# Optimization experiments

Measured on AMD Instinct MI355X. Metric: run time of the kernel, lower is better.

## Reference

```python
import jax, jax.numpy as jnp
import numpy as np
import math

B, S, E = 4, 2048, 1024


def setup_inputs() -> dict:
    key = jax.random.key(0)
    ks = jax.random.split(key, 9)
    x = jax.random.normal(ks[0], (B, S, E), dtype=jnp.float32)
    # causal boolean mask, broadcast over batch: True = keep
    mask = jnp.broadcast_to(jnp.tril(jnp.ones((S, S), dtype=bool)), (B, S, S))
    sc = 1.0 / math.sqrt(E)
    Wq = jax.random.normal(ks[1], (E, E), dtype=jnp.float32) * sc
    bq = jnp.zeros((E,), dtype=jnp.float32)
    Wk = jax.random.normal(ks[2], (E, E), dtype=jnp.float32) * sc
    bk = jnp.zeros((E,), dtype=jnp.float32)
    Wv = jax.random.normal(ks[3], (E, E), dtype=jnp.float32) * sc
    bv = jnp.zeros((E,), dtype=jnp.float32)
    gamma = jnp.ones((E,), dtype=jnp.float32)
    beta = jnp.zeros((E,), dtype=jnp.float32)
    return {"x": x, "mask": mask, "Wq": Wq, "bq": bq, "Wk": Wk, "bk": bk,
            "Wv": Wv, "bv": bv, "gamma": gamma, "beta": beta}


def reference(x, mask, Wq, bq, Wk, bk, Wv, bv, gamma, beta):
    E_ = x.shape[-1]
    q = jnp.einsum('bse,fe->bsf', x, Wq) + bq
    k = jnp.einsum('bse,fe->bsf', x, Wk) + bk
    v = jnp.einsum('bse,fe->bsf', x, Wv) + bv
    scores = jnp.einsum('bqe,bke->bqk', q, k) / jnp.sqrt(jnp.float32(E_))
    scores = jnp.where(mask, scores, -jnp.inf)
    probs = jax.nn.softmax(scores, axis=-1)
    attn = jnp.einsum('bqk,bke->bqe', probs, v)
    y = attn + x
    # LayerNorm over last dim, eps matches torch default 1e-5
    mu = jnp.mean(y, axis=-1, keepdims=True)
    var = jnp.mean(jnp.square(y - mu), axis=-1, keepdims=True)
    return (y - mu) / jnp.sqrt(var + 1e-5) * gamma + beta
```

## Files before the change

kernel.cpp:

```cpp
#include <hip/hip_runtime.h>
#include <hip/hip_bf16.h>
#include <stdint.h>

#define B_ 4
#define S_ 2048
#define E_ 1024
#define BS_ (B_*S_)

using bf16x8 = __attribute__((ext_vector_type(8))) __bf16;
using f32x4  = __attribute__((ext_vector_type(4))) float;

__device__ __forceinline__ unsigned short f2bf(float f) {
  unsigned int u = __float_as_uint(f);
  u += 0x7fffu + ((u >> 16) & 1u);
  return (unsigned short)(u >> 16);
}

__device__ __forceinline__ void gld16(const unsigned short* g, unsigned short* l) {
  __builtin_amdgcn_global_load_lds((__attribute__((address_space(1))) void*)(void*)g,
                                   (__attribute__((address_space(3))) void*)l, 16, 0, 0);
}

__global__ __launch_bounds__(256) void conv_f32_bf16(const float* __restrict__ in,
                                                     unsigned short* __restrict__ out,
                                                     int n4) {
  int i = blockIdx.x * 256 + threadIdx.x;
  if (i >= n4) return;
  const float4 v = ((const float4*)in)[i];
  ushort4 o;
  o.x = f2bf(v.x); o.y = f2bf(v.y); o.z = f2bf(v.z); o.w = f2bf(v.w);
  ((ushort4*)out)[i] = o;
}

__global__ __launch_bounds__(256) void concat_bias(const float* __restrict__ a,
                                                   const float* __restrict__ b,
                                                   const float* __restrict__ c,
                                                   float* __restrict__ o) {
  int i = blockIdx.x * 256 + threadIdx.x;
  if (i >= 3 * E_) return;
  o[i] = (i < E_) ? a[i] : (i < 2 * E_ ? b[i - E_] : c[i - 2 * E_]);
}

template<int EPI>
__global__ __launch_bounds__(256, 2) void gemm_bt(
    const unsigned short* __restrict__ A, const unsigned short* __restrict__ Bm,
    float* __restrict__ Cf, unsigned short* __restrict__ Cb,
    const float* __restrict__ bias,
    int K, int lda, int ldb, int ldc,
    long sA, long sB, long sC, float scale, int causal)
{
  constexpr int BM = 128, BN = 128, BK = 64;
  __shared__ __align__(16) unsigned short As[BM * BK];
  __shared__ __align__(16) unsigned short Bs[BN * BK];
  const int bz = blockIdx.z;
  A  += sA * bz;
  Bm += sB * bz;
  const int m0 = blockIdx.y * BM, n0 = blockIdx.x * BN;
  if (EPI == 1 && causal && n0 >= m0 + BM) return;
  const int kend = (EPI == 2 && causal) ? min(K, m0 + BM) : K;
  const int t = threadIdx.x;
  const int lane = t & 63, wave = t >> 6;
  const int wr = wave >> 1, wc = wave & 1;
  const int q = lane >> 4, r = lane & 15;

  const int srow   = lane >> 3;
  const int schunk = (lane & 7) ^ srow;
  const long ga0 = (long)(m0 + wave * 32 + srow) * lda + schunk * 8;
  const long gb0 = (long)(n0 + wave * 32 + srow) * ldb + schunk * 8;

  f32x4 acc[4][4] = {};

  for (int k0 = 0; k0 < kend; k0 += BK) {
#pragma unroll
    for (int s = 0; s < 4; ++s) {
      gld16(A  + ga0 + (long)s * 8 * lda + k0, &As[(wave * 32 + s * 8) * 64]);
      gld16(Bm + gb0 + (long)s * 8 * ldb + k0, &Bs[(wave * 32 + s * 8) * 64]);
    }
    __syncthreads();
#pragma unroll
    for (int kk = 0; kk < BK; kk += 32) {
      bf16x8 af[4], bfr[4];
      const int cq = (kk >> 3) + q;
#pragma unroll
      for (int i = 0; i < 4; ++i) {
        const int row = wr * 64 + i * 16 + r;
        af[i] = *(const bf16x8*)&As[(row * 8 + (cq ^ (r & 7))) * 8];
      }
#pragma unroll
      for (int j = 0; j < 4; ++j) {
        const int row = wc * 64 + j * 16 + r;
        bfr[j] = *(const bf16x8*)&Bs[(row * 8 + (cq ^ (r & 7))) * 8];
      }
#pragma unroll
      for (int i = 0; i < 4; ++i)
#pragma unroll
        for (int j = 0; j < 4; ++j)
          acc[i][j] = __builtin_amdgcn_mfma_f32_16x16x32_bf16(af[i], bfr[j], acc[i][j], 0, 0, 0);
    }
    __syncthreads();
  }

  if (EPI == 0) Cb += sC * bz; else Cf += sC * bz;
#pragma unroll
  for (int i = 0; i < 4; ++i) {
#pragma unroll
    for (int j = 0; j < 4; ++j) {
      const int col = n0 + wc * 64 + j * 16 + r;
#pragma unroll
      for (int e = 0; e < 4; ++e) {
        const int rowg = m0 + wr * 64 + i * 16 + q * 4 + e;
        float v = acc[i][j][e];
        if (EPI == 0) {
          v += bias[col];
          Cb[(long)rowg * ldc + col] = f2bf(v);
        } else if (EPI == 1) {
          Cf[(long)rowg * ldc + col] = v * scale;
        } else {
          Cf[(long)rowg * ldc + col] = v;
        }
      }
    }
  }
}

__global__ __launch_bounds__(256) void transpose_b(const unsigned short* __restrict__ V,
                                                   unsigned short* __restrict__ Vt, int lda) {
  __shared__ unsigned short tile[32][33];
  const int b = blockIdx.z;
  const unsigned short* Vb = V + (long)b * S_ * lda;
  unsigned short* Vtb = Vt + (long)b * S_ * E_;
  const int e0 = blockIdx.x * 32, j0 = blockIdx.y * 32;
  const int tx = threadIdx.x, ty = threadIdx.y;
#pragma unroll
  for (int i = 0; i < 32; i += 8)
    tile[ty + i][tx] = Vb[(long)(j0 + ty + i) * lda + e0 + tx];
  __syncthreads();
#pragma unroll
  for (int i = 0; i < 32; i += 8)
    Vtb[(long)(e0 + ty + i) * S_ + j0 + tx] = tile[tx][ty + i];
}

__global__ __launch_bounds__(256) void softmax_causal(float* __restrict__ Sc) {
  __shared__ float ex[S_];
  __shared__ float rmax[4], rsum[4];
  const int row = blockIdx.x;
  const int b = row >> 11, ii = row & (S_ - 1);
  float* srow = Sc + (long)b * S_ * S_ + (long)ii * S_;
  unsigned short* prow = (unsigned short*)srow;
  const int len = ii + 1;
  const int t = threadIdx.x;
  const int lane = t & 63, wave = t >> 6;
  float mx = -3.0e38f;
  for (int j = t; j < len; j += 256) { float s = srow[j]; ex[j] = s; mx = fmaxf(mx, s); }
#pragma unroll
  for (int o = 32; o; o >>= 1) mx = fmaxf(mx, __shfl_xor(mx, o));
  if (lane == 0) rmax[wave] = mx;
  __syncthreads();
  mx = fmaxf(fmaxf(rmax[0], rmax[1]), fmaxf(rmax[2], rmax[3]));
  float sum = 0.f;
  for (int j = t; j < len; j += 256) { float e = __expf(ex[j] - mx); ex[j] = e; sum += e; }
#pragma unroll
  for (int o = 32; o; o >>= 1) sum += __shfl_xor(sum, o);
  if (lane == 0) rsum[wave] = sum;
  __syncthreads();
  sum = rsum[0] + rsum[1] + rsum[2] + rsum[3];
  const float inv = 1.0f / sum;
  for (int j = t; j < S_; j += 256)
    prow[j] = (j < len) ? f2bf(ex[j] * inv) : (unsigned short)0;
}

__global__ __launch_bounds__(256) void residual_ln(
    const float* __restrict__ attn, const float* __restrict__ x,
    const float* __restrict__ gamma, const float* __restrict__ beta,
    float* __restrict__ out) {
  __shared__ float rs[4], rs2[4];
  const long row = blockIdx.x;
  const int t = threadIdx.x;
  const int lane = t & 63, wave = t >> 6;
  const float4 a  = ((const float4*)(attn + row * E_))[t];
  const float4 xv = ((const float4*)(x + row * E_))[t];
  const float y0 = a.x + xv.x, y1 = a.y + xv.y, y2 = a.z + xv.z, y3 = a.w + xv.w;
  float s  = y0 + y1 + y2 + y3;
  float s2 = y0 * y0 + y1 * y1 + y2 * y2 + y3 * y3;
#pragma unroll
  for (int o = 32; o; o >>= 1) { s += __shfl_xor(s, o); s2 += __shfl_xor(s2, o); }
  if (lane == 0) { rs[wave] = s; rs2[wave] = s2; }
  __syncthreads();
  s  = rs[0] + rs[1] + rs[2] + rs[3];
  s2 = rs2[0] + rs2[1] + rs2[2] + rs2[3];
  const float mu  = s * (1.0f / E_);
  const float var = s2 * (1.0f / E_) - mu * mu;
  const float inv = rsqrtf(var + 1e-5f);
  const float4 g  = ((const float4*)gamma)[t];
  const float4 be = ((const float4*)beta)[t];
  float4 o;
  o.x = (y0 - mu) * inv * g.x + be.x;
  o.y = (y1 - mu) * inv * g.y + be.y;
  o.z = (y2 - mu) * inv * g.z + be.z;
  o.w = (y3 - mu) * inv * g.w + be.w;
  ((float4*)(out + row * E_))[t] = o;
}

extern "C" void kernel_launch(void* const* d_in, const int* in_sizes, int n_in,
                              void* d_out, int out_size, void* d_ws, size_t ws_size,
                              hipStream_t stream) {
  const float* x  = (const float*)d_in[0];
  const float* Wq = (const float*)d_in[2];
  const float* bq = (const float*)d_in[3];
  const float* Wk = (const float*)d_in[4];
  const float* bk = (const float*)d_in[5];
  const float* Wv = (const float*)d_in[6];
  const float* bv = (const float*)d_in[7];
  const float* gamma = (const float*)d_in[8];
  const float* beta  = (const float*)d_in[9];
  float* out = (float*)d_out;

  char* ws = (char*)d_ws;
  size_t off = 0;
  auto alloc = [&](size_t bytes) { char* p = ws + off; off += (bytes + 255) & ~(size_t)255; return p; };
  unsigned short* xb    = (unsigned short*)alloc((size_t)BS_ * E_ * 2);
  unsigned short* Wqkvb = (unsigned short*)alloc((size_t)3 * E_ * E_ * 2);
  float*          bqkv  = (float*)alloc((size_t)3 * E_ * 4);
  unsigned short* Cqkv  = (unsigned short*)alloc((size_t)BS_ * 3 * E_ * 2);
  unsigned short* Vt    = (unsigned short*)alloc((size_t)BS_ * E_ * 2);
  float*          Sc    = (float*)alloc((size_t)B_ * S_ * S_ * 4);
  float* attn = (float*)Cqkv;

  conv_f32_bf16<<<dim3(BS_ * E_ / 4 / 256), 256, 0, stream>>>(x, xb, BS_ * E_ / 4);
  conv_f32_bf16<<<dim3(E_ * E_ / 4 / 256), 256, 0, stream>>>(Wq, Wqkvb, E_ * E_ / 4);
  conv_f32_bf16<<<dim3(E_ * E_ / 4 / 256), 256, 0, stream>>>(Wk, Wqkvb + E_ * E_, E_ * E_ / 4);
  conv_f32_bf16<<<dim3(E_ * E_ / 4 / 256), 256, 0, stream>>>(Wv, Wqkvb + 2 * E_ * E_, E_ * E_ / 4);
  concat_bias<<<dim3((3 * E_ + 255) / 256), 256, 0, stream>>>(bq, bk, bv, bqkv);

  dim3 g1(3 * E_ / 128, BS_ / 128, 1);
  gemm_bt<0><<<g1, 256, 0, stream>>>(xb, Wqkvb, nullptr, Cqkv, bqkv,
                                     E_, E_, E_, 3 * E_, 0, 0, 0, 1.f, 0);

  transpose_b<<<dim3(E_ / 32, S_ / 32, B_), dim3(32, 8), 0, stream>>>(Cqkv + 2 * E_, Vt, 3 * E_);

  dim3 g2(S_ / 128, S_ / 128, B_);
  gemm_bt<1><<<g2, 256, 0, stream>>>(Cqkv, Cqkv + E_, Sc, nullptr, nullptr,
                                     E_, 3 * E_, 3 * E_, S_,
                                     (long)S_ * 3 * E_, (long)S_ * 3 * E_, (long)S_ * S_,
                                     0.03125f, 1);

  softmax_causal<<<dim3(BS_), 256, 0, stream>>>(Sc);

  dim3 g3(E_ / 128, S_ / 128, B_);
  gemm_bt<2><<<g3, 256, 0, stream>>>((const unsigned short*)Sc, Vt, attn, nullptr, nullptr,
                                     S_, 2 * S_, S_, E_,
                                     (long)2 * S_ * S_, (long)S_ * E_, (long)S_ * E_, 1.f, 1);

  residual_ln<<<dim3(BS_), 256, 0, stream>>>(attn, x, gamma, beta, out);
}
```

Baseline: 320.0 us.

## Store attention scores in bf16 and use wave-per-row softmax with vectorized transpose

The QK^T GEMM now writes scaled scores as bf16 instead of fp32, which halves the score buffer and its traffic. Softmax now gives each row to one wave, holds the values in registers, loads and stores 16 bytes at a time, and no longer needs LDS or block syncs. The V transpose moves to 64x64 tiles with ushort4 accesses. Rounding scores to bf16 before softmax adds precision error in the logits.

```diff
diff --git a/kernel.cpp b/kernel.cpp
--- a/kernel.cpp
+++ b/kernel.cpp
@@ -14,6 +14,9 @@
   unsigned int u = __float_as_uint(f);
   u += 0x7fffu + ((u >> 16) & 1u);
   return (unsigned short)(u >> 16);
+}
+__device__ __forceinline__ float bf2f(unsigned short h) {
+  return __uint_as_float(((unsigned int)h) << 16);
 }
 
 __device__ __forceinline__ void gld16(const unsigned short* g, unsigned short* l) {
@@ -100,7 +103,7 @@
     __syncthreads();
   }
 
-  if (EPI == 0) Cb += sC * bz; else Cf += sC * bz;
+  if (EPI == 2) Cf += sC * bz; else Cb += sC * bz;
 #pragma unroll
   for (int i = 0; i < 4; ++i) {
 #pragma unroll
@@ -114,7 +117,7 @@
           v += bias[col];
           Cb[(long)rowg * ldc + col] = f2bf(v);
         } else if (EPI == 1) {
-          Cf[(long)rowg * ldc + col] = v * scale;
+          Cb[(long)rowg * ldc + col] = f2bf(v * scale);
         } else {
           Cf[(long)rowg * ldc + col] = v;
         }
@@ -125,48 +128,80 @@
 
 __global__ __launch_bounds__(256) void transpose_b(const unsigned short* __restrict__ V,
                                                    unsigned short* __restrict__ Vt, int lda) {
-  __shared__ unsigned short tile[32][33];
+  __shared__ unsigned short tile[64][68];
   const int b = blockIdx.z;
   const unsigned short* Vb = V + (long)b * S_ * lda;
   unsigned short* Vtb = Vt + (long)b * S_ * E_;
-  const int e0 = blockIdx.x * 32, j0 = blockIdx.y * 32;
-  const int tx = threadIdx.x, ty = threadIdx.y;
-#pragma unroll
-  for (int i = 0; i < 32; i += 8)
-    tile[ty + i][tx] = Vb[(long)(j0 + ty + i) * lda + e0 + tx];
+  const int e0 = blockIdx.x * 64, j0 = blockIdx.y * 64;
+  const int t = threadIdx.x;
+#pragma unroll
+  for (int i = 0; i < 4; ++i) {
+    const int c = t + i * 256;
+    const int row = c >> 4, c4 = c & 15;
+    *(ushort4*)&tile[row][c4 * 4] = *(const ushort4*)&Vb[(long)(j0 + row) * lda + e0 + c4 * 4];
+  }
   __syncthreads();
 #pragma unroll
-  for (int i = 0; i < 32; i += 8)
-    Vtb[(long)(e0 + ty + i) * S_ + j0 + tx] = tile[tx][ty + i];
-}
-
-__global__ __launch_bounds__(256) void softmax_causal(float* __restrict__ Sc) {
-  __shared__ float ex[S_];
-  __shared__ float rmax[4], rsum[4];
-  const int row = blockIdx.x;
+  for (int i = 0; i < 4; ++i) {
+    const int c = t + i * 256;
+    const int orow = c >> 4, c4 = c & 15;
+    ushort4 o;
+    o.x = tile[c4 * 4 + 0][orow];
+    o.y = tile[c4 * 4 + 1][orow];
+    o.z = tile[c4 * 4 + 2][orow];
+    o.w = tile[c4 * 4 + 3][orow];
+    *(ushort4*)&Vtb[(long)(e0 + orow) * S_ + j0 + c4 * 4] = o;
+  }
+}
+
+__global__ __launch_bounds__(256) void softmax_causal(unsigned short* __restrict__ Sc) {
+  const int row = blockIdx.x * 4 + (threadIdx.x >> 6);
+  const int lane = threadIdx.x & 63;
   const int b = row >> 11, ii = row & (S_ - 1);
-  float* srow = Sc + (long)b * S_ * S_ + (long)ii * S_;
-  unsigned short* prow = (unsigned short*)srow;
+  unsigned short* prow = Sc + (long)b * S_ * S_ + (long)ii * S_;
   const int len = ii + 1;
-  const int t = threadIdx.x;
-  const int lane = t & 63, wave = t >> 6;
+  float v[32];
+#pragma unroll
+  for (int c = 0; c < 4; ++c) {
+    const int base = (c * 64 + lane) * 8;
+    if (base < len) {
+      const uint4 u = *(const uint4*)&prow[base];
+      const unsigned int w[4] = {u.x, u.y, u.z, u.w};
+#pragma unroll
+      for (int e = 0; e < 8; ++e) {
+        const unsigned short h = (unsigned short)(w[e >> 1] >> ((e & 1) * 16));
+        v[c * 8 + e] = (base + e < len) ? bf2f(h) : -3.0e38f;
+      }
+    } else {
+#pragma unroll
+      for (int e = 0; e < 8; ++e) v[c * 8 + e] = -3.0e38f;
+    }
+  }
   float mx = -3.0e38f;
-  for (int j = t; j < len; j += 256) { float s = srow[j]; ex[j] = s; mx = fmaxf(mx, s); }
+#pragma unroll
+  for (int i = 0; i < 32; ++i) mx = fmaxf(mx, v[i]);
 #pragma unroll
   for (int o = 32; o; o >>= 1) mx = fmaxf(mx, __shfl_xor(mx, o));
-  if (lane == 0) rmax[wave] = mx;
-  __syncthreads();
-  mx = fmaxf(fmaxf(rmax[0], rmax[1]), fmaxf(rmax[2], rmax[3]));
   float sum = 0.f;
-  for (int j = t; j < len; j += 256) { float e = __expf(ex[j] - mx); ex[j] = e; sum += e; }
+#pragma unroll
+  for (int i = 0; i < 32; ++i) { v[i] = __expf(v[i] - mx); sum += v[i]; }
 #pragma unroll
   for (int o = 32; o; o >>= 1) sum += __shfl_xor(sum, o);
-  if (lane == 0) rsum[wave] = sum;
-  __syncthreads();
-  sum = rsum[0] + rsum[1] + rsum[2] + rsum[3];
   const float inv = 1.0f / sum;
-  for (int j = t; j < S_; j += 256)
-    prow[j] = (j < len) ? f2bf(ex[j] * inv) : (unsigned short)0;
+#pragma unroll
+  for (int c = 0; c < 4; ++c) {
+    const int base = (c * 64 + lane) * 8;
+    uint4 u;
+    unsigned int w[4];
+#pragma unroll
+    for (int p = 0; p < 4; ++p) {
+      const unsigned short lo = f2bf(v[c * 8 + p * 2] * inv);
+      const unsigned short hi = f2bf(v[c * 8 + p * 2 + 1] * inv);
+      w[p] = (unsigned int)lo | ((unsigned int)hi << 16);
+    }
+    u.x = w[0]; u.y = w[1]; u.z = w[2]; u.w = w[3];
+    *(uint4*)&prow[base] = u;
+  }
 }
 
 __global__ __launch_bounds__(256) void residual_ln(
@@ -223,7 +258,7 @@
   float*          bqkv  = (float*)alloc((size_t)3 * E_ * 4);
   unsigned short* Cqkv  = (unsigned short*)alloc((size_t)BS_ * 3 * E_ * 2);
   unsigned short* Vt    = (unsigned short*)alloc((size_t)BS_ * E_ * 2);
-  float*          Sc    = (float*)alloc((size_t)B_ * S_ * S_ * 4);
+  unsigned short* Sc    = (unsigned short*)alloc((size_t)B_ * S_ * S_ * 2);
   float* attn = (float*)Cqkv;
 
   conv_f32_bf16<<<dim3(BS_ * E_ / 4 / 256), 256, 0, stream>>>(x, xb, BS_ * E_ / 4);
@@ -236,20 +271,20 @@
   gemm_bt<0><<<g1, 256, 0, stream>>>(xb, Wqkvb, nullptr, Cqkv, bqkv,
                                      E_, E_, E_, 3 * E_, 0, 0, 0, 1.f, 0);
 
-  transpose_b<<<dim3(E_ / 32, S_ / 32, B_), dim3(32, 8), 0, stream>>>(Cqkv + 2 * E_, Vt, 3 * E_);
+  transpose_b<<<dim3(E_ / 64, S_ / 64, B_), 256, 0, stream>>>(Cqkv + 2 * E_, Vt, 3 * E_);
 
   dim3 g2(S_ / 128, S_ / 128, B_);
-  gemm_bt<1><<<g2, 256, 0, stream>>>(Cqkv, Cqkv + E_, Sc, nullptr, nullptr,
+  gemm_bt<1><<<g2, 256, 0, stream>>>(Cqkv, Cqkv + E_, nullptr, Sc, nullptr,
                                      E_, 3 * E_, 3 * E_, S_,
                                      (long)S_ * 3 * E_, (long)S_ * 3 * E_, (long)S_ * S_,
                                      0.03125f, 1);
 
-  softmax_causal<<<dim3(BS_), 256, 0, stream>>>(Sc);
+  softmax_causal<<<dim3(BS_ / 4), 256, 0, stream>>>(Sc);
 
   dim3 g3(E_ / 128, S_ / 128, B_);
-  gemm_bt<2><<<g3, 256, 0, stream>>>((const unsigned short*)Sc, Vt, attn, nullptr, nullptr,
-                                     S_, 2 * S_, S_, E_,
-                                     (long)2 * S_ * S_, (long)S_ * E_, (long)S_ * E_, 1.f, 1);
+  gemm_bt<2><<<g3, 256, 0, stream>>>(Sc, Vt, attn, nullptr, nullptr,
+                                     S_, S_, S_, E_,
+                                     (long)S_ * S_, (long)S_ * E_, (long)S_ * E_, 1.f, 1);
 
   residual_ln<<<dim3(BS_), 256, 0, stream>>>(attn, x, gamma, beta, out);
 }
```

Measured after the change: 306.5 us. 4.2% less time.
